# Optimization experiments

Hardware: AMD Instinct MI355X
Metric: run time of the kernel (lower is better)

Reference implementation:

```python
import jax, jax.numpy as jnp
import numpy as np

WS = (8, 8)          # window size
NUM_HEADS = 16
C = 512
B_ = 2048            # batch * num_windows
NW = 256             # num_windows per image (mask dim)
N = WS[0] * WS[1]    # tokens per window = 64


def _relative_position_index():
    coords = np.stack(np.meshgrid(np.arange(WS[0]), np.arange(WS[1]), indexing='ij'))  # [2,Wh,Ww]
    flat = coords.reshape(2, -1)                         # [2,N]
    rel = flat[:, :, None] - flat[:, None, :]            # [2,N,N]
    rel = rel.transpose(1, 2, 0).astype(np.int32)        # [N,N,2]
    rel[..., 0] += WS[0] - 1
    rel[..., 1] += WS[1] - 1
    rel[..., 0] *= 2 * WS[1] - 1
    return jnp.asarray(rel.sum(-1))                      # [N,N] in [0, 225)


def setup_inputs() -> dict:
    key = jax.random.key(0)
    ks = jax.random.split(key, 8)
    return {
        'x': jax.random.normal(ks[0], (B_, N, C), jnp.float32),
        'mask': jax.random.normal(ks[1], (NW, N, N), jnp.float32),
        'qkv_w': jax.random.normal(ks[2], (3 * C, C), jnp.float32) * 0.02,
        'q_bias': jax.random.normal(ks[3], (C,), jnp.float32) * 0.02,
        'v_bias': jax.random.normal(ks[4], (C,), jnp.float32) * 0.02,
        'rpb_table': jax.random.normal(ks[5], ((2 * WS[0] - 1) * (2 * WS[1] - 1), NUM_HEADS), jnp.float32) * 0.02,
        'proj_w': jax.random.normal(ks[6], (C, C), jnp.float32) * 0.02,
        'proj_b': jax.random.normal(ks[7], (C,), jnp.float32) * 0.02,
        'rel_index': _relative_position_index(),
    }


def reference(x, mask, qkv_w, q_bias, v_bias, rpb_table, proj_w, proj_b, rel_index):
    Bw, n, c = x.shape
    h = NUM_HEADS
    d = c // h
    # qkv with bias = [q_bias, 0, v_bias]
    qkv_b = jnp.concatenate([q_bias, jnp.zeros_like(v_bias), v_bias])
    qkv = x @ qkv_w.T + qkv_b                               # [B_,N,3C]
    qkv = qkv.reshape(Bw, n, 3, h, d).transpose(2, 0, 3, 1, 4)
    q, k, v = qkv[0], qkv[1], qkv[2]                        # each [B_,h,N,d]
    scale = d ** -0.5
    attn = jnp.einsum('bhnd,bhmd->bhnm', q * scale, k)      # [B_,h,N,N]
    # gathered relative position bias
    rpb = rpb_table[rel_index.reshape(-1)].reshape(n, n, h).transpose(2, 0, 1)  # [h,N,N]
    attn = attn + rpb[None]
    nW = mask.shape[0]
    attn = attn.reshape(Bw // nW, nW, h, n, n) + mask[None, :, None]
    attn = jax.nn.softmax(attn.reshape(Bw, h, n, n), axis=-1)
    out = jnp.einsum('bhnm,bhmd->bhnd', attn, v)            # [B_,h,N,d]
    out = out.transpose(0, 2, 1, 3).reshape(Bw, n, c)
    return out @ proj_w.T + proj_b
```

## Files before the change

### kernel.cpp

```cpp
#include <hip/hip_runtime.h>

typedef short s16x8 __attribute__((ext_vector_type(8)));
typedef float f32x4 __attribute__((ext_vector_type(4)));

__device__ __forceinline__ unsigned short f2bf(float f) {
    unsigned int u = __builtin_bit_cast(unsigned int, f);
    u += 0x7fffu + ((u >> 16) & 1u);
    return (unsigned short)(u >> 16);
}

__device__ __forceinline__ void gload16(const void* g, void* l) {
    __builtin_amdgcn_global_load_lds(
        (const __attribute__((address_space(1))) unsigned int*)g,
        (__attribute__((address_space(3))) unsigned int*)l,
        16, 0, 0);
}

__global__ void cast_bf16_kernel(const float* __restrict__ src,
                                 unsigned short* __restrict__ dst, int n4) {
    int i = blockIdx.x * 256 + threadIdx.x;
    if (i >= n4) return;
    float4 v = ((const float4*)src)[i];
    ushort4 o;
    o.x = f2bf(v.x); o.y = f2bf(v.y); o.z = f2bf(v.z); o.w = f2bf(v.w);
    ((ushort4*)dst)[i] = o;
}

__global__ void rpb_kernel(const float* __restrict__ table,
                           const int* __restrict__ rel,
                           float* __restrict__ rpb) {
    int t = blockIdx.x * 64 + threadIdx.x;
    int idx = rel[t];
#pragma unroll
    for (int h = 0; h < 16; ++h)
        rpb[h * 4096 + t] = table[idx * 16 + h];
}

template <int MODE, int NCOLS>
__global__ __launch_bounds__(256) void gemm_bt(
    const unsigned short* __restrict__ A, const unsigned short* __restrict__ B,
    const float* __restrict__ bq, const float* __restrict__ bv,
    unsigned short* __restrict__ qb, unsigned short* __restrict__ kb,
    unsigned short* __restrict__ vtb,
    const float* __restrict__ pb, float* __restrict__ out) {
    constexpr int SMEM_SHORTS = (MODE == 0) ? 16384 : 8192;
    __shared__ unsigned short smem[SMEM_SHORTS];
    unsigned short* Al = smem;
    unsigned short* Bl = smem + 4096;

    constexpr int NBN = NCOLS / 128;
    const int bm = blockIdx.x / NBN;
    const int bn = blockIdx.x % NBN;
    const int t = threadIdx.x;
    const int wave = t >> 6, lane = t & 63;
    const int ln = lane & 15, hk = lane >> 4;
    const int wr = (wave >> 1) * 64, wc = (wave & 1) * 64;

    const f32x4 zero = {0.f, 0.f, 0.f, 0.f};
    f32x4 acc[4][4];
#pragma unroll
    for (int i = 0; i < 4; ++i)
#pragma unroll
        for (int j = 0; j < 4; ++j) acc[i][j] = zero;

    const unsigned short* Ab = A + (size_t)bm * 128 * 512;
    const unsigned short* Bb = B + (size_t)bn * 128 * 512;
    const int row = t >> 2, cg = t & 3;

    for (int k0 = 0; k0 < 512; k0 += 32) {
        gload16(Ab + (size_t)row * 512 + k0 + cg * 8, &Al[(wave * 64) * 8]);
        gload16(Ab + (size_t)(row + 64) * 512 + k0 + cg * 8, &Al[(256 + wave * 64) * 8]);
        gload16(Bb + (size_t)row * 512 + k0 + cg * 8, &Bl[(wave * 64) * 8]);
        gload16(Bb + (size_t)(row + 64) * 512 + k0 + cg * 8, &Bl[(256 + wave * 64) * 8]);
        __syncthreads();
        s16x8 af[4], bf[4];
#pragma unroll
        for (int i = 0; i < 4; ++i)
            af[i] = *(const s16x8*)&Al[(wr + i * 16 + ln) * 32 + hk * 8];
#pragma unroll
        for (int j = 0; j < 4; ++j)
            bf[j] = *(const s16x8*)&Bl[(wc + j * 16 + ln) * 32 + hk * 8];
#pragma unroll
        for (int i = 0; i < 4; ++i)
#pragma unroll
            for (int j = 0; j < 4; ++j)
                acc[i][j] = __builtin_amdgcn_mfma_f32_16x16x32_bf16(af[i], bf[j], acc[i][j], 0, 0, 0);
        __syncthreads();
    }

    if constexpr (MODE == 0) {
        const int which = bn >> 2;
#pragma unroll
        for (int i = 0; i < 4; ++i) {
#pragma unroll
            for (int j = 0; j < 4; ++j) {
                const int colT = wc + j * 16 + ln;
                const int nn = bn * 128 + colT;
                const int rem = nn & 511;
                float bias = 0.f;
                if (which == 0) bias = bq[rem];
                else if (which == 2) bias = bv[rem];
                const int g = colT >> 3, cl = colT & 7;
#pragma unroll
                for (int r = 0; r < 4; ++r) {
                    const int rowT = wr + i * 16 + hk * 4 + r;
                    const int key = (rowT >> 3) & 7;
                    smem[rowT * 128 + ((g ^ key) << 3) + cl] = f2bf(acc[i][j][r] + bias);
                }
            }
        }
        __syncthreads();
        const int bb = bm * 2;
        if (which < 2) {
            unsigned short* dst0 = (which == 0) ? qb : kb;
#pragma unroll
            for (int c = 0; c < 8; ++c) {
                const int bl = c >> 2, hl = c & 3;
                const int head = (bn & 3) * 4 + hl;
                const int rowT = bl * 64 + (t >> 2);
                const int colT = hl * 32 + (t & 3) * 8;
                const int g = colT >> 3, key = (rowT >> 3) & 7;
                s16x8 val = *(const s16x8*)&smem[rowT * 128 + ((g ^ key) << 3)];
                *(s16x8*)(dst0 + ((size_t)((bb + bl) * 16 + head)) * 2048 + (size_t)t * 8) = val;
            }
        } else {
#pragma unroll
            for (int c = 0; c < 8; ++c) {
                const int bl = c >> 2, hl = c & 3;
                const int head = (bn & 3) * 4 + hl;
                const int dd = t >> 3, tok0 = (t & 7) * 8;
                const int colT = hl * 32 + dd;
                const int g = colT >> 3, cl = colT & 7;
                s16x8 val;
#pragma unroll
                for (int ii = 0; ii < 8; ++ii) {
                    const int rowT = bl * 64 + tok0 + ii;
                    const int key = (rowT >> 3) & 7;
                    val[ii] = (short)smem[rowT * 128 + ((g ^ key) << 3) + cl];
                }
                *(s16x8*)(vtb + ((size_t)((bb + bl) * 16 + head)) * 2048 + (size_t)t * 8) = val;
            }
        }
    } else {
#pragma unroll
        for (int i = 0; i < 4; ++i) {
            const int mbase = bm * 128 + wr + i * 16 + hk * 4;
#pragma unroll
            for (int j = 0; j < 4; ++j) {
                const int nn = bn * 128 + wc + j * 16 + ln;
                const float bias = pb[nn];
#pragma unroll
                for (int r = 0; r < 4; ++r)
                    out[(size_t)(mbase + r) * NCOLS + nn] = acc[i][j][r] + bias;
            }
        }
    }
}

__global__ __launch_bounds__(256) void attn_kernel(
    const unsigned short* __restrict__ qbuf, const unsigned short* __restrict__ kbuf,
    const unsigned short* __restrict__ vtbuf, const float* __restrict__ rpb,
    const float* __restrict__ mask, unsigned short* __restrict__ aout) {
    __shared__ unsigned short ql[64 * 32];
    __shared__ unsigned short kl[64 * 32];
    __shared__ unsigned short vl[32 * 64];
    __shared__ unsigned short plds[64 * 64];

    const int bh = blockIdx.x;
    const int b = bh >> 4, head = bh & 15;
    const int wmask = b & 255;
    const int t = threadIdx.x, wave = t >> 6, lane = t & 63;
    const int ln = lane & 15, hk = lane >> 4;

    const size_t base = (size_t)bh * 2048;
    gload16(qbuf + base + t * 8, &ql[wave * 512]);
    gload16(kbuf + base + t * 8, &kl[wave * 512]);
    gload16(vtbuf + base + t * 8, &vl[wave * 512]);
    __syncthreads();

    const f32x4 zero = {0.f, 0.f, 0.f, 0.f};
    s16x8 aq = *(const s16x8*)&ql[(wave * 16 + ln) * 32 + hk * 8];
    f32x4 sc[4];
#pragma unroll
    for (int j = 0; j < 4; ++j) {
        s16x8 bk = *(const s16x8*)&kl[(j * 16 + ln) * 32 + hk * 8];
        sc[j] = __builtin_amdgcn_mfma_f32_16x16x32_bf16(aq, bk, zero, 0, 0, 0);
    }

    const float scale = 0.17677669529663687f;
    const float* rpb_h = rpb + head * 4096;
    const float* msk = mask + wmask * 4096;

    float p[4][4];
#pragma unroll
    for (int r = 0; r < 4; ++r) {
        const int i = wave * 16 + hk * 4 + r;
        float v[4], m = -1e30f;
#pragma unroll
        for (int j = 0; j < 4; ++j) {
            const int c = j * 16 + ln;
            v[j] = sc[j][r] * scale + rpb_h[i * 64 + c] + msk[i * 64 + c];
            m = fmaxf(m, v[j]);
        }
        for (int off = 1; off < 16; off <<= 1) m = fmaxf(m, __shfl_xor(m, off));
        float s = 0.f;
#pragma unroll
        for (int j = 0; j < 4; ++j) { v[j] = __expf(v[j] - m); s += v[j]; }
        for (int off = 1; off < 16; off <<= 1) s += __shfl_xor(s, off);
        const float inv = 1.f / s;
#pragma unroll
        for (int j = 0; j < 4; ++j) p[r][j] = v[j] * inv;
    }
#pragma unroll
    for (int r = 0; r < 4; ++r)
#pragma unroll
        for (int j = 0; j < 4; ++j)
            plds[(wave * 16 + hk * 4 + r) * 64 + j * 16 + ln] = f2bf(p[r][j]);
    __syncthreads();

    f32x4 o[2] = {zero, zero};
#pragma unroll
    for (int kt = 0; kt < 2; ++kt) {
        s16x8 ap = *(const s16x8*)&plds[(wave * 16 + ln) * 64 + kt * 32 + hk * 8];
#pragma unroll
        for (int nt = 0; nt < 2; ++nt) {
            s16x8 bvf = *(const s16x8*)&vl[(nt * 16 + ln) * 64 + kt * 32 + hk * 8];
            o[nt] = __builtin_amdgcn_mfma_f32_16x16x32_bf16(ap, bvf, o[nt], 0, 0, 0);
        }
    }
#pragma unroll
    for (int nt = 0; nt < 2; ++nt)
#pragma unroll
        for (int r = 0; r < 4; ++r) {
            const int i = wave * 16 + hk * 4 + r;
            const int dd = nt * 16 + ln;
            aout[((size_t)(b * 64 + i)) * 512 + head * 32 + dd] = f2bf(o[nt][r]);
        }
}

extern "C" void kernel_launch(void* const* d_in, const int* in_sizes, int n_in,
                              void* d_out, int out_size, void* d_ws, size_t ws_size,
                              hipStream_t stream) {
    const float* x      = (const float*)d_in[0];
    const float* mask   = (const float*)d_in[1];
    const float* qkv_w  = (const float*)d_in[2];
    const float* q_bias = (const float*)d_in[3];
    const float* v_bias = (const float*)d_in[4];
    const float* rpb_t  = (const float*)d_in[5];
    const float* proj_w = (const float*)d_in[6];
    const float* proj_b = (const float*)d_in[7];
    const int*   rel    = (const int*)d_in[8];
    float* out = (float*)d_out;

    char* ws = (char*)d_ws;
    unsigned short* xbf   = (unsigned short*)ws;
    unsigned short* qbuf  = (unsigned short*)(ws + 0x08000000);
    unsigned short* kbuf  = (unsigned short*)(ws + 0x10000000);
    unsigned short* vtbuf = (unsigned short*)(ws + 0x18000000);
    unsigned short* wqkv  = (unsigned short*)(ws + 0x20000000);
    unsigned short* wproj = (unsigned short*)(ws + 0x20180000);
    float*          rpb   = (float*)(ws + 0x20200000);
    unsigned short* aout  = xbf;

    cast_bf16_kernel<<<65536, 256, 0, stream>>>(x, xbf, 16777216);
    cast_bf16_kernel<<<768, 256, 0, stream>>>(qkv_w, wqkv, 196608);
    cast_bf16_kernel<<<256, 256, 0, stream>>>(proj_w, wproj, 65536);
    rpb_kernel<<<64, 64, 0, stream>>>(rpb_t, rel, rpb);

    gemm_bt<0, 1536><<<1024 * 12, 256, 0, stream>>>(
        xbf, wqkv, q_bias, v_bias, qbuf, kbuf, vtbuf, nullptr, nullptr);

    attn_kernel<<<32768, 256, 0, stream>>>(qbuf, kbuf, vtbuf, rpb, mask, aout);

    gemm_bt<1, 512><<<1024 * 4, 256, 0, stream>>>(
        aout, wproj, nullptr, nullptr, nullptr, nullptr, nullptr, proj_b, out);
}
```

Baseline: 1.081 ms.

## Swap MFMA operands to vectorize epilogue stores and remap GEMM block order

The GEMM and attention epilogues swap the MFMA A/B operands so each lane holds four consecutive output columns. This lets them write ushort4/float4 vectors directly to global memory instead of scalar stores or an LDS transpose staging pass. The QKV GEMM drops its 32KB shared staging buffer, which may raise occupancy. A block-index remap spreads consecutive workgroups across 8 XCD-sized chunks, aiming at better L2 locality. The V path still writes transposed data with ushort4 stores at a stride, which may leave those writes poorly coalesced.

```diff
diff --git a/kernel.cpp b/kernel.cpp
--- a/kernel.cpp
+++ b/kernel.cpp
@@ -36,6 +36,39 @@
         rpb[h * 4096 + t] = table[idx * 16 + h];
 }
 
+template <bool SW>
+__device__ __forceinline__ void kloop128(const unsigned short* __restrict__ Ab,
+                                         const unsigned short* __restrict__ Bb,
+                                         unsigned short* Al, unsigned short* Bl,
+                                         int t, int wave, int ln, int hk,
+                                         int wr, int wc, f32x4 (&acc)[4][4]) {
+    const int row = t >> 2, cg = t & 3;
+    for (int k0 = 0; k0 < 512; k0 += 32) {
+        gload16(Ab + (size_t)row * 512 + k0 + cg * 8, &Al[wave * 512]);
+        gload16(Ab + (size_t)(row + 64) * 512 + k0 + cg * 8, &Al[2048 + wave * 512]);
+        gload16(Bb + (size_t)row * 512 + k0 + cg * 8, &Bl[wave * 512]);
+        gload16(Bb + (size_t)(row + 64) * 512 + k0 + cg * 8, &Bl[2048 + wave * 512]);
+        __syncthreads();
+        s16x8 af[4], bf[4];
+#pragma unroll
+        for (int i = 0; i < 4; ++i)
+            af[i] = *(const s16x8*)&Al[(wr + i * 16 + ln) * 32 + hk * 8];
+#pragma unroll
+        for (int j = 0; j < 4; ++j)
+            bf[j] = *(const s16x8*)&Bl[(wc + j * 16 + ln) * 32 + hk * 8];
+#pragma unroll
+        for (int i = 0; i < 4; ++i)
+#pragma unroll
+            for (int j = 0; j < 4; ++j) {
+                if constexpr (SW)
+                    acc[j][i] = __builtin_amdgcn_mfma_f32_16x16x32_bf16(bf[j], af[i], acc[j][i], 0, 0, 0);
+                else
+                    acc[i][j] = __builtin_amdgcn_mfma_f32_16x16x32_bf16(af[i], bf[j], acc[i][j], 0, 0, 0);
+            }
+        __syncthreads();
+    }
+}
+
 template <int MODE, int NCOLS>
 __global__ __launch_bounds__(256) void gemm_bt(
     const unsigned short* __restrict__ A, const unsigned short* __restrict__ B,
@@ -43,14 +76,15 @@
     unsigned short* __restrict__ qb, unsigned short* __restrict__ kb,
     unsigned short* __restrict__ vtb,
     const float* __restrict__ pb, float* __restrict__ out) {
-    constexpr int SMEM_SHORTS = (MODE == 0) ? 16384 : 8192;
-    __shared__ unsigned short smem[SMEM_SHORTS];
+    __shared__ unsigned short smem[8192];
     unsigned short* Al = smem;
     unsigned short* Bl = smem + 4096;
 
     constexpr int NBN = NCOLS / 128;
-    const int bm = blockIdx.x / NBN;
-    const int bn = blockIdx.x % NBN;
+    const unsigned int cpx = gridDim.x >> 3;
+    const unsigned int wg = (blockIdx.x & 7u) * cpx + (blockIdx.x >> 3);
+    const int bm = wg / NBN;
+    const int bn = wg % NBN;
     const int t = threadIdx.x;
     const int wave = t >> 6, lane = t & 63;
     const int ln = lane & 15, hk = lane >> 4;
@@ -65,93 +99,69 @@
 
     const unsigned short* Ab = A + (size_t)bm * 128 * 512;
     const unsigned short* Bb = B + (size_t)bn * 128 * 512;
-    const int row = t >> 2, cg = t & 3;
-
-    for (int k0 = 0; k0 < 512; k0 += 32) {
-        gload16(Ab + (size_t)row * 512 + k0 + cg * 8, &Al[(wave * 64) * 8]);
-        gload16(Ab + (size_t)(row + 64) * 512 + k0 + cg * 8, &Al[(256 + wave * 64) * 8]);
-        gload16(Bb + (size_t)row * 512 + k0 + cg * 8, &Bl[(wave * 64) * 8]);
-        gload16(Bb + (size_t)(row + 64) * 512 + k0 + cg * 8, &Bl[(256 + wave * 64) * 8]);
-        __syncthreads();
-        s16x8 af[4], bf[4];
-#pragma unroll
-        for (int i = 0; i < 4; ++i)
-            af[i] = *(const s16x8*)&Al[(wr + i * 16 + ln) * 32 + hk * 8];
-#pragma unroll
-        for (int j = 0; j < 4; ++j)
-            bf[j] = *(const s16x8*)&Bl[(wc + j * 16 + ln) * 32 + hk * 8];
-#pragma unroll
-        for (int i = 0; i < 4; ++i)
-#pragma unroll
-            for (int j = 0; j < 4; ++j)
-                acc[i][j] = __builtin_amdgcn_mfma_f32_16x16x32_bf16(af[i], bf[j], acc[i][j], 0, 0, 0);
-        __syncthreads();
-    }
-
-    if constexpr (MODE == 0) {
+
+    if constexpr (MODE == 1) {
+        kloop128<true>(Ab, Bb, Al, Bl, t, wave, ln, hk, wr, wc, acc);
+#pragma unroll
+        for (int j = 0; j < 4; ++j) {
+            const int nn0 = bn * 128 + wc + j * 16 + hk * 4;
+            const float4 b4 = *(const float4*)&pb[nn0];
+#pragma unroll
+            for (int i = 0; i < 4; ++i) {
+                const int m = bm * 128 + wr + i * 16 + ln;
+                float4 o4;
+                o4.x = acc[j][i][0] + b4.x;
+                o4.y = acc[j][i][1] + b4.y;
+                o4.z = acc[j][i][2] + b4.z;
+                o4.w = acc[j][i][3] + b4.w;
+                *(float4*)(out + (size_t)m * NCOLS + nn0) = o4;
+            }
+        }
+    } else {
         const int which = bn >> 2;
-#pragma unroll
-        for (int i = 0; i < 4; ++i) {
-#pragma unroll
-            for (int j = 0; j < 4; ++j) {
-                const int colT = wc + j * 16 + ln;
-                const int nn = bn * 128 + colT;
-                const int rem = nn & 511;
-                float bias = 0.f;
-                if (which == 0) bias = bq[rem];
-                else if (which == 2) bias = bv[rem];
-                const int g = colT >> 3, cl = colT & 7;
-#pragma unroll
-                for (int r = 0; r < 4; ++r) {
-                    const int rowT = wr + i * 16 + hk * 4 + r;
-                    const int key = (rowT >> 3) & 7;
-                    smem[rowT * 128 + ((g ^ key) << 3) + cl] = f2bf(acc[i][j][r] + bias);
-                }
-            }
-        }
-        __syncthreads();
         const int bb = bm * 2;
         if (which < 2) {
+            kloop128<true>(Ab, Bb, Al, Bl, t, wave, ln, hk, wr, wc, acc);
             unsigned short* dst0 = (which == 0) ? qb : kb;
 #pragma unroll
-            for (int c = 0; c < 8; ++c) {
-                const int bl = c >> 2, hl = c & 3;
-                const int head = (bn & 3) * 4 + hl;
-                const int rowT = bl * 64 + (t >> 2);
-                const int colT = hl * 32 + (t & 3) * 8;
-                const int g = colT >> 3, key = (rowT >> 3) & 7;
-                s16x8 val = *(const s16x8*)&smem[rowT * 128 + ((g ^ key) << 3)];
-                *(s16x8*)(dst0 + ((size_t)((bb + bl) * 16 + head)) * 2048 + (size_t)t * 8) = val;
+            for (int j = 0; j < 4; ++j) {
+                const int colT0 = wc + j * 16 + hk * 4;
+                const int rem0 = (bn * 128 + colT0) & 511;
+                float4 b4 = {0.f, 0.f, 0.f, 0.f};
+                if (which == 0) b4 = *(const float4*)&bq[rem0];
+                const int head = rem0 >> 5;
+                const int dd0 = rem0 & 31;
+#pragma unroll
+                for (int i = 0; i < 4; ++i) {
+                    const int tokL = wr + i * 16 + ln;
+                    const size_t bh = (size_t)((bb + (tokL >> 6)) * 16 + head);
+                    ushort4 pk;
+                    pk.x = f2bf(acc[j][i][0] + b4.x);
+                    pk.y = f2bf(acc[j][i][1] + b4.y);
+                    pk.z = f2bf(acc[j][i][2] + b4.z);
+                    pk.w = f2bf(acc[j][i][3] + b4.w);
+                    *(ushort4*)(dst0 + bh * 2048 + (size_t)(tokL & 63) * 32 + dd0) = pk;
+                }
             }
         } else {
-#pragma unroll
-            for (int c = 0; c < 8; ++c) {
-                const int bl = c >> 2, hl = c & 3;
-                const int head = (bn & 3) * 4 + hl;
-                const int dd = t >> 3, tok0 = (t & 7) * 8;
-                const int colT = hl * 32 + dd;
-                const int g = colT >> 3, cl = colT & 7;
-                s16x8 val;
-#pragma unroll
-                for (int ii = 0; ii < 8; ++ii) {
-                    const int rowT = bl * 64 + tok0 + ii;
-                    const int key = (rowT >> 3) & 7;
-                    val[ii] = (short)smem[rowT * 128 + ((g ^ key) << 3) + cl];
+            kloop128<false>(Ab, Bb, Al, Bl, t, wave, ln, hk, wr, wc, acc);
+#pragma unroll
+            for (int i = 0; i < 4; ++i) {
+                const int tok0L = wr + i * 16 + hk * 4;
+                const size_t bhbase = (size_t)(bb + (tok0L >> 6)) * 16;
+                const int tok0 = tok0L & 63;
+#pragma unroll
+                for (int j = 0; j < 4; ++j) {
+                    const int rem = (bn * 128 + wc + j * 16 + ln) & 511;
+                    const float bias = bv[rem];
+                    const int head = rem >> 5, dd = rem & 31;
+                    ushort4 pk;
+                    pk.x = f2bf(acc[i][j][0] + bias);
+                    pk.y = f2bf(acc[i][j][1] + bias);
+                    pk.z = f2bf(acc[i][j][2] + bias);
+                    pk.w = f2bf(acc[i][j][3] + bias);
+                    *(ushort4*)(vtb + (bhbase + head) * 2048 + (size_t)dd * 64 + tok0) = pk;
                 }
-                *(s16x8*)(vtb + ((size_t)((bb + bl) * 16 + head)) * 2048 + (size_t)t * 8) = val;
-            }
-        }
-    } else {
-#pragma unroll
-        for (int i = 0; i < 4; ++i) {
-            const int mbase = bm * 128 + wr + i * 16 + hk * 4;
-#pragma unroll
-            for (int j = 0; j < 4; ++j) {
-                const int nn = bn * 128 + wc + j * 16 + ln;
-                const float bias = pb[nn];
-#pragma unroll
-                for (int r = 0; r < 4; ++r)
-                    out[(size_t)(mbase + r) * NCOLS + nn] = acc[i][j][r] + bias;
             }
         }
     }
@@ -218,24 +228,24 @@
             plds[(wave * 16 + hk * 4 + r) * 64 + j * 16 + ln] = f2bf(p[r][j]);
     __syncthreads();
 
-    f32x4 o[2] = {zero, zero};
+    f32x4 o2[2] = {zero, zero};
 #pragma unroll
     for (int kt = 0; kt < 2; ++kt) {
         s16x8 ap = *(const s16x8*)&plds[(wave * 16 + ln) * 64 + kt * 32 + hk * 8];
 #pragma unroll
         for (int nt = 0; nt < 2; ++nt) {
             s16x8 bvf = *(const s16x8*)&vl[(nt * 16 + ln) * 64 + kt * 32 + hk * 8];
-            o[nt] = __builtin_amdgcn_mfma_f32_16x16x32_bf16(ap, bvf, o[nt], 0, 0, 0);
-        }
-    }
-#pragma unroll
-    for (int nt = 0; nt < 2; ++nt)
-#pragma unroll
-        for (int r = 0; r < 4; ++r) {
-            const int i = wave * 16 + hk * 4 + r;
-            const int dd = nt * 16 + ln;
-            aout[((size_t)(b * 64 + i)) * 512 + head * 32 + dd] = f2bf(o[nt][r]);
-        }
+            o2[nt] = __builtin_amdgcn_mfma_f32_16x16x32_bf16(bvf, ap, o2[nt], 0, 0, 0);
+        }
+    }
+#pragma unroll
+    for (int nt = 0; nt < 2; ++nt) {
+        ushort4 pk;
+        pk.x = f2bf(o2[nt][0]); pk.y = f2bf(o2[nt][1]);
+        pk.z = f2bf(o2[nt][2]); pk.w = f2bf(o2[nt][3]);
+        *(ushort4*)(aout + ((size_t)(b * 64 + wave * 16 + ln)) * 512
+                    + head * 32 + nt * 16 + hk * 4) = pk;
+    }
 }
 
 extern "C" void kernel_launch(void* const* d_in, const int* in_sizes, int n_in,
```

After: 1.137 ms. 1.05x slower.
